# Kernel optimization log

Hardware: AMD Instinct MI355X
Metric: run time of the kernel (lower is better)

Reference implementation:

```python
import jax, jax.numpy as jnp
import numpy as np

N_NODES = 25000
N_EDGES = 800000
NUM_GRAPHS = 512
EMB = 128
OUT_EMB = 256
NUM_RADIAL = 6
NUM_DENSE = 3
NUM_TARGETS = 12


def setup_inputs() -> dict:
    key = jax.random.key(0)
    ks = jax.random.split(key, 10)
    m = jax.random.normal(ks[0], (N_EDGES, EMB), dtype=jnp.float32)
    rbf = jax.random.normal(ks[1], (N_EDGES, NUM_RADIAL), dtype=jnp.float32)
    edge_src = jax.random.randint(ks[2], (N_EDGES,), 0, N_NODES, dtype=jnp.int32)
    node2graph = jnp.sort(jax.random.randint(ks[3], (N_NODES,), 0, NUM_GRAPHS, dtype=jnp.int32))
    w_rbf = jax.random.normal(ks[4], (NUM_RADIAL, EMB), dtype=jnp.float32) * 0.4
    w_up = jax.random.normal(ks[5], (EMB, OUT_EMB), dtype=jnp.float32) * 0.08
    w_dense = jax.random.normal(ks[6], (NUM_DENSE, OUT_EMB, OUT_EMB), dtype=jnp.float32) * 0.06
    b_dense = jax.random.normal(ks[7], (NUM_DENSE, OUT_EMB), dtype=jnp.float32) * 0.01
    w_final = jax.random.normal(ks[8], (OUT_EMB, NUM_TARGETS), dtype=jnp.float32) * 0.05
    return {"m": m, "rbf": rbf, "edge_src": edge_src, "node2graph": node2graph,
            "w_rbf": w_rbf, "w_up": w_up, "w_dense": w_dense, "b_dense": b_dense,
            "w_final": w_final, "num_graphs": NUM_GRAPHS}


def reference(m, rbf, edge_src, node2graph, w_rbf, w_up, w_dense, b_dense, w_final, num_graphs):
    n_nodes = node2graph.shape[0]
    # edge: tmp = m * dense_rbf(rbf)   [E, emb]
    tmp = m * (rbf @ w_rbf)
    # reverse graph + copy_e/sum == scatter-sum per-edge tmp into original src node
    t = jax.ops.segment_sum(tmp, edge_src, num_segments=n_nodes)  # [N, emb]
    # up projection (no bias)
    t = t @ w_up  # [N, out_emb]
    # dense layers with swish activation
    for i in range(w_dense.shape[0]):
        t = jax.nn.silu(t @ w_dense[i] + b_dense[i])
    # final projection (no bias)
    t = t @ w_final  # [N, num_targets]
    # extensive readout: per-graph sum over nodes
    return jax.ops.segment_sum(t, node2graph, num_segments=num_graphs)  # [G, num_targets]
```

## Files before the change

### kernel.cpp

```cpp
#include <hip/hip_runtime.h>
#include <hip/hip_bf16.h>
#include <math.h>

#define EMB 128
#define OUT 256
#define RAD 6
#define NDL 3
#define NTGT 12
#define MT 32
#define S 264

typedef __attribute__((ext_vector_type(8))) short short8;
typedef __attribute__((ext_vector_type(4))) float floatx4;

__device__ inline short f2bf(float x) {
    __hip_bfloat16 h = __float2bfloat16(x);
    return *reinterpret_cast<short*>(&h);
}

__device__ inline unsigned pack2bf(float x, float y) {
    unsigned a = (unsigned short)f2bf(x);
    unsigned b = (unsigned short)f2bf(y);
    return a | (b << 16);
}


__global__ void hist_kernel(const int* __restrict__ src, int* __restrict__ counts, int E) {
    int i = blockIdx.x * blockDim.x + threadIdx.x;
    if (i < E) atomicAdd(&counts[src[i]], 1);
}

__global__ void scan_kernel(const int* __restrict__ counts, int* __restrict__ offs,
                            int* __restrict__ cursor, int N) {
    __shared__ int sums[1024];
    int tid = threadIdx.x;
    int chunk = (N + 1023) / 1024;
    int beg = tid * chunk;
    int end = min(beg + chunk, N);
    int s = 0;
    for (int i = beg; i < end; i++) s += counts[i];
    int mysum = s;
    sums[tid] = s;
    __syncthreads();
    for (int off = 1; off < 1024; off <<= 1) {
        int add = (tid >= off) ? sums[tid - off] : 0;
        __syncthreads();
        sums[tid] += add;
        __syncthreads();
    }
    int prefix = sums[tid] - mysum;
    for (int i = beg; i < end; i++) {
        int c = counts[i];
        offs[i] = prefix;
        cursor[i] = prefix;
        prefix += c;
    }
    if (tid == 0) offs[N] = sums[1023];
}

__global__ void scatter_kernel(const int* __restrict__ src, int* __restrict__ cursor,
                               int* __restrict__ eids, int E) {
    int i = blockIdx.x * blockDim.x + threadIdx.x;
    if (i < E) {
        int pos = atomicAdd(&cursor[src[i]], 1);
        eids[pos] = i;
    }
}


__global__ void prep_kernel(const float* __restrict__ w_up, const float* __restrict__ w_dense,
                            const float* __restrict__ w_final,
                            short* __restrict__ w_upT, short* __restrict__ w_dT,
                            short* __restrict__ w_fT) {
    const int T1 = OUT * EMB;
    const int T2 = NDL * OUT * OUT;
    const int T3 = 16 * OUT;
    int total = T1 + T2 + T3;
    for (int i = blockIdx.x * blockDim.x + threadIdx.x; i < total; i += gridDim.x * blockDim.x) {
        if (i < T1) {
            int n = i >> 7, k = i & 127;
            w_upT[i] = f2bf(w_up[k * OUT + n]);
        } else if (i < T1 + T2) {
            int j = i - T1;
            int l = j >> 16, o = (j >> 8) & 255, k = j & 255;
            w_dT[j] = f2bf(w_dense[(l << 16) + (k << 8) + o]);
        } else {
            int j = i - T1 - T2;
            int t = j >> 8, k = j & 255;
            w_fT[j] = (t < NTGT) ? f2bf(w_final[k * NTGT + t]) : (short)0;
        }
    }
}


__global__ __launch_bounds__(256) void fused_kernel(
    const float* __restrict__ m, const float* __restrict__ rbf,
    const float* __restrict__ w_rbf,
    const int* __restrict__ offs, const int* __restrict__ eids,
    const short* __restrict__ w_upT, const short* __restrict__ w_dT,
    const float* __restrict__ b_dense, const short* __restrict__ w_fT,
    const int* __restrict__ node2graph, float* __restrict__ out, int N) {

    __shared__ short sA[2][MT * S];

    const int tid = threadIdx.x;
    const int n0 = blockIdx.x * MT;
    const int wave = tid >> 6, lane = tid & 63;
    const int lo = lane & 15;
    const int quad = lane >> 4;
    const int kq = quad * 8;
    const int wcol = wave * 64;

    float2 wq[RAD];
#pragma unroll
    for (int r = 0; r < RAD; r++) wq[r] = *(const float2*)&w_rbf[r * EMB + 2 * lane];

#pragma unroll 1
    for (int s = 0; s < 8; s++) {
        const int r = wave * 8 + s;
        const int n = n0 + r;
        float ax = 0.f, ay = 0.f;
        if (n < N) {
            const int b = offs[n], e = offs[n + 1];
            int i = b;
            for (; i + 4 <= e; i += 4) {
                int ev[4];
                float2 mv[4];
                float2 rv[4][3];
#pragma unroll
                for (int j = 0; j < 4; j++) ev[j] = eids[i + j];
#pragma unroll
                for (int j = 0; j < 4; j++) {
                    const float* rb = &rbf[(size_t)ev[j] * RAD];
                    rv[j][0] = *(const float2*)&rb[0];
                    rv[j][1] = *(const float2*)&rb[2];
                    rv[j][2] = *(const float2*)&rb[4];
                    mv[j] = *(const float2*)&m[(size_t)ev[j] * EMB + 2 * lane];
                }
#pragma unroll
                for (int j = 0; j < 4; j++) {
                    float cx = wq[0].x * rv[j][0].x + wq[1].x * rv[j][0].y
                             + wq[2].x * rv[j][1].x + wq[3].x * rv[j][1].y
                             + wq[4].x * rv[j][2].x + wq[5].x * rv[j][2].y;
                    float cy = wq[0].y * rv[j][0].x + wq[1].y * rv[j][0].y
                             + wq[2].y * rv[j][1].x + wq[3].y * rv[j][1].y
                             + wq[4].y * rv[j][2].x + wq[5].y * rv[j][2].y;
                    ax += mv[j].x * cx;
                    ay += mv[j].y * cy;
                }
            }
            for (; i < e; i++) {
                int e0 = eids[i];
                const float* rb = &rbf[(size_t)e0 * RAD];
                float2 p0 = *(const float2*)&rb[0];
                float2 p1 = *(const float2*)&rb[2];
                float2 p2 = *(const float2*)&rb[4];
                float2 m0 = *(const float2*)&m[(size_t)e0 * EMB + 2 * lane];
                float cx = wq[0].x * p0.x + wq[1].x * p0.y + wq[2].x * p1.x
                         + wq[3].x * p1.y + wq[4].x * p2.x + wq[5].x * p2.y;
                float cy = wq[0].y * p0.x + wq[1].y * p0.y + wq[2].y * p1.x
                         + wq[3].y * p1.y + wq[4].y * p2.x + wq[5].y * p2.y;
                ax += m0.x * cx;
                ay += m0.y * cy;
            }
        }
        *(unsigned*)&sA[0][r * S + 2 * lane] = pack2bf(ax, ay);
    }
    __syncthreads();

    auto layer = [&](int cur, int K, const short* __restrict__ Bt,
                     const float* __restrict__ bias, bool act) {
        floatx4 acc[2][4];
#pragma unroll
        for (int mt = 0; mt < 2; mt++)
#pragma unroll
            for (int nt = 0; nt < 4; nt++)
                acc[mt][nt] = floatx4{0.f, 0.f, 0.f, 0.f};

        for (int kc = 0; kc < K; kc += 32) {
            short8 a0 = *(const short8*)&sA[cur][(lo) * S + kc + kq];
            short8 a1 = *(const short8*)&sA[cur][(16 + lo) * S + kc + kq];
#pragma unroll
            for (int nt = 0; nt < 4; nt++) {
                int n = wcol + nt * 16 + lo;
                short8 b = *(const short8*)&Bt[(size_t)n * K + kc + kq];
                acc[0][nt] = __builtin_amdgcn_mfma_f32_16x16x32_bf16(a0, b, acc[0][nt], 0, 0, 0);
                acc[1][nt] = __builtin_amdgcn_mfma_f32_16x16x32_bf16(a1, b, acc[1][nt], 0, 0, 0);
            }
        }

        float bv[4];
#pragma unroll
        for (int nt = 0; nt < 4; nt++) bv[nt] = bias ? bias[wcol + nt * 16 + lo] : 0.f;

        short* dst = sA[cur ^ 1];
#pragma unroll
        for (int mt = 0; mt < 2; mt++)
#pragma unroll
            for (int nt = 0; nt < 4; nt++) {
                int n = wcol + nt * 16 + lo;
#pragma unroll
                for (int i = 0; i < 4; i++) {
                    int mrow = mt * 16 + quad * 4 + i;
                    float x = acc[mt][nt][i] + bv[nt];
                    if (act) x = x / (1.f + __expf(-x));
                    dst[mrow * S + n] = f2bf(x);
                }
            }
        __syncthreads();
    };

    layer(0, EMB, w_upT, nullptr, false);
    layer(1, OUT, w_dT + 0 * OUT * OUT, b_dense + 0 * OUT, true);
    layer(0, OUT, w_dT + 1 * OUT * OUT, b_dense + 1 * OUT, true);
    layer(1, OUT, w_dT + 2 * OUT * OUT, b_dense + 2 * OUT, true);

    if (wave == 0) {
        floatx4 facc[2];
        facc[0] = floatx4{0.f, 0.f, 0.f, 0.f};
        facc[1] = floatx4{0.f, 0.f, 0.f, 0.f};
        for (int kc = 0; kc < OUT; kc += 32) {
            short8 a0 = *(const short8*)&sA[0][(lo) * S + kc + kq];
            short8 a1 = *(const short8*)&sA[0][(16 + lo) * S + kc + kq];
            short8 b = *(const short8*)&w_fT[lo * OUT + kc + kq];
            facc[0] = __builtin_amdgcn_mfma_f32_16x16x32_bf16(a0, b, facc[0], 0, 0, 0);
            facc[1] = __builtin_amdgcn_mfma_f32_16x16x32_bf16(a1, b, facc[1], 0, 0, 0);
        }
        if (lo < NTGT) {
#pragma unroll
            for (int mt = 0; mt < 2; mt++)
#pragma unroll
                for (int i = 0; i < 4; i++) {
                    int node = n0 + mt * 16 + quad * 4 + i;
                    if (node < N)
                        atomicAdd(&out[node2graph[node] * NTGT + lo], facc[mt][i]);
                }
        }
    }
}


extern "C" void kernel_launch(void* const* d_in, const int* in_sizes, int n_in,
                              void* d_out, int out_size, void* d_ws, size_t ws_size,
                              hipStream_t stream) {
    const float* m        = (const float*)d_in[0];
    const float* rbf      = (const float*)d_in[1];
    const int*   edge_src = (const int*)d_in[2];
    const int*   node2g   = (const int*)d_in[3];
    const float* w_rbf    = (const float*)d_in[4];
    const float* w_up     = (const float*)d_in[5];
    const float* w_dense  = (const float*)d_in[6];
    const float* b_dense  = (const float*)d_in[7];
    const float* w_final  = (const float*)d_in[8];

    int E = in_sizes[2];
    int N = in_sizes[3];
    float* out = (float*)d_out;

    char* p = (char*)d_ws;
    auto alloc = [&](size_t bytes) {
        char* r = p;
        p += (bytes + 255) & ~(size_t)255;
        return r;
    };
    int*   counts = (int*)alloc((size_t)N * 4);
    int*   offs   = (int*)alloc((size_t)(N + 1) * 4);
    int*   cursor = (int*)alloc((size_t)N * 4);
    int*   eids   = (int*)alloc((size_t)E * 4);
    short* w_upT  = (short*)alloc((size_t)OUT * EMB * 2);
    short* w_dT   = (short*)alloc((size_t)NDL * OUT * OUT * 2);
    short* w_fT   = (short*)alloc((size_t)16 * OUT * 2);

    hipMemsetAsync(counts, 0, (size_t)N * 4, stream);
    hipMemsetAsync(d_out, 0, (size_t)out_size * 4, stream);

    prep_kernel<<<512, 256, 0, stream>>>(w_up, w_dense, w_final, w_upT, w_dT, w_fT);
    hist_kernel<<<(E + 255) / 256, 256, 0, stream>>>(edge_src, counts, E);
    scan_kernel<<<1, 1024, 0, stream>>>(counts, offs, cursor, N);
    scatter_kernel<<<(E + 255) / 256, 256, 0, stream>>>(edge_src, cursor, eids, E);
    fused_kernel<<<(N + MT - 1) / MT, 256, 0, stream>>>(m, rbf, w_rbf, offs, eids,
                                                        w_upT, w_dT, b_dense, w_fT,
                                                        node2g, out, N);
}
```

Before: 811.7 us.

## Split fused kernel into per-node edge gather and separate MLP chain kernel

```diff
diff --git a/kernel.cpp b/kernel.cpp
--- a/kernel.cpp
+++ b/kernel.cpp
@@ -93,78 +93,139 @@
 }
 
 
-__global__ __launch_bounds__(256) void fused_kernel(
+__global__ __launch_bounds__(256) void gather_kernel(
     const float* __restrict__ m, const float* __restrict__ rbf,
     const float* __restrict__ w_rbf,
     const int* __restrict__ offs, const int* __restrict__ eids,
+    __hip_bfloat16* __restrict__ t0, int N) {
+
+    __shared__ float sRed[4][32][4];
+
+    const int n = blockIdx.x;
+    const int tid = threadIdx.x;
+    const int g = tid >> 5;
+    const int c = tid & 31;
+    const int wave = tid >> 6;
+
+    float4 wq[RAD];
+#pragma unroll
+    for (int r = 0; r < RAD; r++) wq[r] = *(const float4*)&w_rbf[r * EMB + 4 * c];
+
+    const int b = offs[n], e = offs[n + 1];
+    float ax = 0.f, ay = 0.f, az = 0.f, aw = 0.f;
+
+    int i = b + g;
+    for (; i + 24 < e; i += 32) {
+        int ev[4];
+        ev[0] = eids[i];
+        ev[1] = eids[i + 8];
+        ev[2] = eids[i + 16];
+        ev[3] = eids[i + 24];
+        float2 rv[4][3];
+        float4 mv[4];
+#pragma unroll
+        for (int j = 0; j < 4; j++) {
+            const float* rb = &rbf[(size_t)ev[j] * RAD];
+            rv[j][0] = *(const float2*)&rb[0];
+            rv[j][1] = *(const float2*)&rb[2];
+            rv[j][2] = *(const float2*)&rb[4];
+            mv[j] = *(const float4*)&m[(size_t)ev[j] * EMB + 4 * c];
+        }
+#pragma unroll
+        for (int j = 0; j < 4; j++) {
+            float cx = wq[0].x * rv[j][0].x + wq[1].x * rv[j][0].y
+                     + wq[2].x * rv[j][1].x + wq[3].x * rv[j][1].y
+                     + wq[4].x * rv[j][2].x + wq[5].x * rv[j][2].y;
+            float cy = wq[0].y * rv[j][0].x + wq[1].y * rv[j][0].y
+                     + wq[2].y * rv[j][1].x + wq[3].y * rv[j][1].y
+                     + wq[4].y * rv[j][2].x + wq[5].y * rv[j][2].y;
+            float cz = wq[0].z * rv[j][0].x + wq[1].z * rv[j][0].y
+                     + wq[2].z * rv[j][1].x + wq[3].z * rv[j][1].y
+                     + wq[4].z * rv[j][2].x + wq[5].z * rv[j][2].y;
+            float cw = wq[0].w * rv[j][0].x + wq[1].w * rv[j][0].y
+                     + wq[2].w * rv[j][1].x + wq[3].w * rv[j][1].y
+                     + wq[4].w * rv[j][2].x + wq[5].w * rv[j][2].y;
+            ax += mv[j].x * cx;
+            ay += mv[j].y * cy;
+            az += mv[j].z * cz;
+            aw += mv[j].w * cw;
+        }
+    }
+    for (; i < e; i += 8) {
+        int e0 = eids[i];
+        const float* rb = &rbf[(size_t)e0 * RAD];
+        float2 p0 = *(const float2*)&rb[0];
+        float2 p1 = *(const float2*)&rb[2];
+        float2 p2 = *(const float2*)&rb[4];
+        float4 m0 = *(const float4*)&m[(size_t)e0 * EMB + 4 * c];
+        float cx = wq[0].x * p0.x + wq[1].x * p0.y + wq[2].x * p1.x
+                 + wq[3].x * p1.y + wq[4].x * p2.x + wq[5].x * p2.y;
+        float cy = wq[0].y * p0.x + wq[1].y * p0.y + wq[2].y * p1.x
+                 + wq[3].y * p1.y + wq[4].y * p2.x + wq[5].y * p2.y;
+        float cz = wq[0].z * p0.x + wq[1].z * p0.y + wq[2].z * p1.x
+                 + wq[3].z * p1.y + wq[4].z * p2.x + wq[5].z * p2.y;
+        float cw = wq[0].w * p0.x + wq[1].w * p0.y + wq[2].w * p1.x
+                 + wq[3].w * p1.y + wq[4].w * p2.x + wq[5].w * p2.y;
+        ax += m0.x * cx;
+        ay += m0.y * cy;
+        az += m0.z * cz;
+        aw += m0.w * cw;
+    }
+
+    ax += __shfl_xor(ax, 32);
+    ay += __shfl_xor(ay, 32);
+    az += __shfl_xor(az, 32);
+    aw += __shfl_xor(aw, 32);
+
+    if ((tid & 63) < 32) {
+        float4 v = {ax, ay, az, aw};
+        *(float4*)&sRed[wave][c][0] = v;
+    }
+    __syncthreads();
+    if (tid < 32) {
+        float4 v0 = *(const float4*)&sRed[0][c][0];
+        float4 v1 = *(const float4*)&sRed[1][c][0];
+        float4 v2 = *(const float4*)&sRed[2][c][0];
+        float4 v3 = *(const float4*)&sRed[3][c][0];
+        float rx = v0.x + v1.x + v2.x + v3.x;
+        float ry = v0.y + v1.y + v2.y + v3.y;
+        float rz = v0.z + v1.z + v2.z + v3.z;
+        float rw = v0.w + v1.w + v2.w + v3.w;
+        unsigned lo = pack2bf(rx, ry);
+        unsigned hi = pack2bf(rz, rw);
+        uint2 pk = {lo, hi};
+        *(uint2*)((short*)t0 + (size_t)n * EMB + 4 * c) = pk;
+    }
+}
+
+
+__global__ __launch_bounds__(256) void chain_kernel(
+    const __hip_bfloat16* __restrict__ t0,
     const short* __restrict__ w_upT, const short* __restrict__ w_dT,
     const float* __restrict__ b_dense, const short* __restrict__ w_fT,
     const int* __restrict__ node2graph, float* __restrict__ out, int N) {
 
     __shared__ short sA[2][MT * S];
 
-    const int tid = threadIdx.x;
-    const int n0 = blockIdx.x * MT;
-    const int wave = tid >> 6, lane = tid & 63;
-    const int lo = lane & 15;
-    const int quad = lane >> 4;
-    const int kq = quad * 8;
-    const int wcol = wave * 64;
-
-    float2 wq[RAD];
-#pragma unroll
-    for (int r = 0; r < RAD; r++) wq[r] = *(const float2*)&w_rbf[r * EMB + 2 * lane];
-
-#pragma unroll 1
-    for (int s = 0; s < 8; s++) {
-        const int r = wave * 8 + s;
-        const int n = n0 + r;
-        float ax = 0.f, ay = 0.f;
-        if (n < N) {
-            const int b = offs[n], e = offs[n + 1];
-            int i = b;
-            for (; i + 4 <= e; i += 4) {
-                int ev[4];
-                float2 mv[4];
-                float2 rv[4][3];
-#pragma unroll
-                for (int j = 0; j < 4; j++) ev[j] = eids[i + j];
-#pragma unroll
-                for (int j = 0; j < 4; j++) {
-                    const float* rb = &rbf[(size_t)ev[j] * RAD];
-                    rv[j][0] = *(const float2*)&rb[0];
-                    rv[j][1] = *(const float2*)&rb[2];
-                    rv[j][2] = *(const float2*)&rb[4];
-                    mv[j] = *(const float2*)&m[(size_t)ev[j] * EMB + 2 * lane];
-                }
-#pragma unroll
-                for (int j = 0; j < 4; j++) {
-                    float cx = wq[0].x * rv[j][0].x + wq[1].x * rv[j][0].y
-                             + wq[2].x * rv[j][1].x + wq[3].x * rv[j][1].y
-                             + wq[4].x * rv[j][2].x + wq[5].x * rv[j][2].y;
-                    float cy = wq[0].y * rv[j][0].x + wq[1].y * rv[j][0].y
-                             + wq[2].y * rv[j][1].x + wq[3].y * rv[j][1].y
-                             + wq[4].y * rv[j][2].x + wq[5].y * rv[j][2].y;
-                    ax += mv[j].x * cx;
-                    ay += mv[j].y * cy;
-                }
-            }
-            for (; i < e; i++) {
-                int e0 = eids[i];
-                const float* rb = &rbf[(size_t)e0 * RAD];
-                float2 p0 = *(const float2*)&rb[0];
-                float2 p1 = *(const float2*)&rb[2];
-                float2 p2 = *(const float2*)&rb[4];
-                float2 m0 = *(const float2*)&m[(size_t)e0 * EMB + 2 * lane];
-                float cx = wq[0].x * p0.x + wq[1].x * p0.y + wq[2].x * p1.x
-                         + wq[3].x * p1.y + wq[4].x * p2.x + wq[5].x * p2.y;
-                float cy = wq[0].y * p0.x + wq[1].y * p0.y + wq[2].y * p1.x
-                         + wq[3].y * p1.y + wq[4].y * p2.x + wq[5].y * p2.y;
-                ax += m0.x * cx;
-                ay += m0.y * cy;
-            }
-        }
-        *(unsigned*)&sA[0][r * S + 2 * lane] = pack2bf(ax, ay);
+    int tid = threadIdx.x;
+    int n0 = blockIdx.x * MT;
+    int wave = tid >> 6, lane = tid & 63;
+    int lo = lane & 15;
+    int quad = lane >> 4;
+    int kq = quad * 8;
+    int wcol = wave * 64;
+
+    {
+        int r = tid >> 3;
+        int c = (tid & 7) * 16;
+        uint4 v0 = {0, 0, 0, 0}, v1 = {0, 0, 0, 0};
+        if (n0 + r < N) {
+            const uint4* src = (const uint4*)((const short*)t0 + (size_t)(n0 + r) * EMB + c);
+            v0 = src[0];
+            v1 = src[1];
+        }
+        *(uint4*)&sA[0][r * S + c] = v0;
+        *(uint4*)&sA[0][r * S + c + 8] = v1;
     }
     __syncthreads();
 
@@ -267,6 +328,7 @@
     int*   offs   = (int*)alloc((size_t)(N + 1) * 4);
     int*   cursor = (int*)alloc((size_t)N * 4);
     int*   eids   = (int*)alloc((size_t)E * 4);
+    __hip_bfloat16* t0 = (__hip_bfloat16*)alloc((size_t)N * EMB * 2);
     short* w_upT  = (short*)alloc((size_t)OUT * EMB * 2);
     short* w_dT   = (short*)alloc((size_t)NDL * OUT * OUT * 2);
     short* w_fT   = (short*)alloc((size_t)16 * OUT * 2);
@@ -278,7 +340,7 @@
     hist_kernel<<<(E + 255) / 256, 256, 0, stream>>>(edge_src, counts, E);
     scan_kernel<<<1, 1024, 0, stream>>>(counts, offs, cursor, N);
     scatter_kernel<<<(E + 255) / 256, 256, 0, stream>>>(edge_src, cursor, eids, E);
-    fused_kernel<<<(N + MT - 1) / MT, 256, 0, stream>>>(m, rbf, w_rbf, offs, eids,
-                                                        w_upT, w_dT, b_dense, w_fT,
-                                                        node2g, out, N);
-}
+    gather_kernel<<<N, 256, 0, stream>>>(m, rbf, w_rbf, offs, eids, t0, N);
+    chain_kernel<<<(N + MT - 1) / MT, 256, 0, stream>>>(t0, w_upT, w_dT, b_dense,
+                                                        w_fT, node2g, out, N);
+}
```

Result: faster. 779.7 us (-3.9%).

## Replace CSR sort-based gather with atomic scatter-add into fp32 node buffer

Applied to the files above, without the earlier changes.

```diff
diff --git a/kernel.cpp b/kernel.cpp
--- a/kernel.cpp
+++ b/kernel.cpp
@@ -22,49 +22,6 @@
     unsigned a = (unsigned short)f2bf(x);
     unsigned b = (unsigned short)f2bf(y);
     return a | (b << 16);
-}
-
-
-__global__ void hist_kernel(const int* __restrict__ src, int* __restrict__ counts, int E) {
-    int i = blockIdx.x * blockDim.x + threadIdx.x;
-    if (i < E) atomicAdd(&counts[src[i]], 1);
-}
-
-__global__ void scan_kernel(const int* __restrict__ counts, int* __restrict__ offs,
-                            int* __restrict__ cursor, int N) {
-    __shared__ int sums[1024];
-    int tid = threadIdx.x;
-    int chunk = (N + 1023) / 1024;
-    int beg = tid * chunk;
-    int end = min(beg + chunk, N);
-    int s = 0;
-    for (int i = beg; i < end; i++) s += counts[i];
-    int mysum = s;
-    sums[tid] = s;
-    __syncthreads();
-    for (int off = 1; off < 1024; off <<= 1) {
-        int add = (tid >= off) ? sums[tid - off] : 0;
-        __syncthreads();
-        sums[tid] += add;
-        __syncthreads();
-    }
-    int prefix = sums[tid] - mysum;
-    for (int i = beg; i < end; i++) {
-        int c = counts[i];
-        offs[i] = prefix;
-        cursor[i] = prefix;
-        prefix += c;
-    }
-    if (tid == 0) offs[N] = sums[1023];
-}
-
-__global__ void scatter_kernel(const int* __restrict__ src, int* __restrict__ cursor,
-                               int* __restrict__ eids, int E) {
-    int i = blockIdx.x * blockDim.x + threadIdx.x;
-    if (i < E) {
-        int pos = atomicAdd(&cursor[src[i]], 1);
-        eids[pos] = i;
-    }
 }
 
 
@@ -93,78 +50,98 @@
 }
 
 
-__global__ __launch_bounds__(256) void fused_kernel(
+__global__ __launch_bounds__(256) void edge_kernel(
     const float* __restrict__ m, const float* __restrict__ rbf,
-    const float* __restrict__ w_rbf,
-    const int* __restrict__ offs, const int* __restrict__ eids,
+    const float* __restrict__ w_rbf, const int* __restrict__ edge_src,
+    float* __restrict__ t0, int E) {
+
+    const int lane = threadIdx.x & 63;
+    const int wave = threadIdx.x >> 6;
+
+    float2 wq[RAD];
+#pragma unroll
+    for (int r = 0; r < RAD; r++) wq[r] = *(const float2*)&w_rbf[r * EMB + 2 * lane];
+
+    const int base = (blockIdx.x * 4 + wave) * 4;
+    if (base >= E) return;
+
+    if (base + 4 <= E) {
+        int sv[4];
+        float2 mv[4];
+        float2 r0[4], r1[4], r2[4];
+#pragma unroll
+        for (int j = 0; j < 4; j++) sv[j] = edge_src[base + j];
+#pragma unroll
+        for (int j = 0; j < 4; j++) {
+            const float* rb = &rbf[(size_t)(base + j) * RAD];
+            r0[j] = *(const float2*)&rb[0];
+            r1[j] = *(const float2*)&rb[2];
+            r2[j] = *(const float2*)&rb[4];
+            mv[j] = *(const float2*)&m[(size_t)(base + j) * EMB + 2 * lane];
+        }
+#pragma unroll
+        for (int j = 0; j < 4; j++) {
+            float cx = wq[0].x * r0[j].x + wq[1].x * r0[j].y
+                     + wq[2].x * r1[j].x + wq[3].x * r1[j].y
+                     + wq[4].x * r2[j].x + wq[5].x * r2[j].y;
+            float cy = wq[0].y * r0[j].x + wq[1].y * r0[j].y
+                     + wq[2].y * r1[j].x + wq[3].y * r1[j].y
+                     + wq[4].y * r2[j].x + wq[5].y * r2[j].y;
+            float* dst = &t0[(size_t)sv[j] * EMB + 2 * lane];
+            atomicAdd(&dst[0], mv[j].x * cx);
+            atomicAdd(&dst[1], mv[j].y * cy);
+        }
+    } else {
+        for (int i = base; i < E; i++) {
+            int s0 = edge_src[i];
+            const float* rb = &rbf[(size_t)i * RAD];
+            float2 p0 = *(const float2*)&rb[0];
+            float2 p1 = *(const float2*)&rb[2];
+            float2 p2 = *(const float2*)&rb[4];
+            float2 m0 = *(const float2*)&m[(size_t)i * EMB + 2 * lane];
+            float cx = wq[0].x * p0.x + wq[1].x * p0.y + wq[2].x * p1.x
+                     + wq[3].x * p1.y + wq[4].x * p2.x + wq[5].x * p2.y;
+            float cy = wq[0].y * p0.x + wq[1].y * p0.y + wq[2].y * p1.x
+                     + wq[3].y * p1.y + wq[4].y * p2.x + wq[5].y * p2.y;
+            float* dst = &t0[(size_t)s0 * EMB + 2 * lane];
+            atomicAdd(&dst[0], m0.x * cx);
+            atomicAdd(&dst[1], m0.y * cy);
+        }
+    }
+}
+
+
+__global__ __launch_bounds__(256) void chain_kernel(
+    const float* __restrict__ t0,
     const short* __restrict__ w_upT, const short* __restrict__ w_dT,
     const float* __restrict__ b_dense, const short* __restrict__ w_fT,
     const int* __restrict__ node2graph, float* __restrict__ out, int N) {
 
     __shared__ short sA[2][MT * S];
 
-    const int tid = threadIdx.x;
-    const int n0 = blockIdx.x * MT;
-    const int wave = tid >> 6, lane = tid & 63;
-    const int lo = lane & 15;
-    const int quad = lane >> 4;
-    const int kq = quad * 8;
-    const int wcol = wave * 64;
-
-    float2 wq[RAD];
-#pragma unroll
-    for (int r = 0; r < RAD; r++) wq[r] = *(const float2*)&w_rbf[r * EMB + 2 * lane];
-
-#pragma unroll 1
-    for (int s = 0; s < 8; s++) {
-        const int r = wave * 8 + s;
-        const int n = n0 + r;
-        float ax = 0.f, ay = 0.f;
-        if (n < N) {
-            const int b = offs[n], e = offs[n + 1];
-            int i = b;
-            for (; i + 4 <= e; i += 4) {
-                int ev[4];
-                float2 mv[4];
-                float2 rv[4][3];
-#pragma unroll
-                for (int j = 0; j < 4; j++) ev[j] = eids[i + j];
-#pragma unroll
-                for (int j = 0; j < 4; j++) {
-                    const float* rb = &rbf[(size_t)ev[j] * RAD];
-                    rv[j][0] = *(const float2*)&rb[0];
-                    rv[j][1] = *(const float2*)&rb[2];
-                    rv[j][2] = *(const float2*)&rb[4];
-                    mv[j] = *(const float2*)&m[(size_t)ev[j] * EMB + 2 * lane];
-                }
-#pragma unroll
-                for (int j = 0; j < 4; j++) {
-                    float cx = wq[0].x * rv[j][0].x + wq[1].x * rv[j][0].y
-                             + wq[2].x * rv[j][1].x + wq[3].x * rv[j][1].y
-                             + wq[4].x * rv[j][2].x + wq[5].x * rv[j][2].y;
-                    float cy = wq[0].y * rv[j][0].x + wq[1].y * rv[j][0].y
-                             + wq[2].y * rv[j][1].x + wq[3].y * rv[j][1].y
-                             + wq[4].y * rv[j][2].x + wq[5].y * rv[j][2].y;
-                    ax += mv[j].x * cx;
-                    ay += mv[j].y * cy;
-                }
-            }
-            for (; i < e; i++) {
-                int e0 = eids[i];
-                const float* rb = &rbf[(size_t)e0 * RAD];
-                float2 p0 = *(const float2*)&rb[0];
-                float2 p1 = *(const float2*)&rb[2];
-                float2 p2 = *(const float2*)&rb[4];
-                float2 m0 = *(const float2*)&m[(size_t)e0 * EMB + 2 * lane];
-                float cx = wq[0].x * p0.x + wq[1].x * p0.y + wq[2].x * p1.x
-                         + wq[3].x * p1.y + wq[4].x * p2.x + wq[5].x * p2.y;
-                float cy = wq[0].y * p0.x + wq[1].y * p0.y + wq[2].y * p1.x
-                         + wq[3].y * p1.y + wq[4].y * p2.x + wq[5].y * p2.y;
-                ax += m0.x * cx;
-                ay += m0.y * cy;
-            }
-        }
-        *(unsigned*)&sA[0][r * S + 2 * lane] = pack2bf(ax, ay);
+    int tid = threadIdx.x;
+    int n0 = blockIdx.x * MT;
+    int wave = tid >> 6, lane = tid & 63;
+    int lo = lane & 15;
+    int quad = lane >> 4;
+    int kq = quad * 8;
+    int wcol = wave * 64;
+
+    {
+        int r = tid >> 3;
+        int c = (tid & 7) * 16;
+        float4 v0 = {0, 0, 0, 0}, v1 = v0, v2 = v0, v3 = v0;
+        if (n0 + r < N) {
+            const float4* src = (const float4*)(t0 + (size_t)(n0 + r) * EMB + c);
+            v0 = src[0]; v1 = src[1]; v2 = src[2]; v3 = src[3];
+        }
+        uint4 pk0, pk1;
+        pk0.x = pack2bf(v0.x, v0.y); pk0.y = pack2bf(v0.z, v0.w);
+        pk0.z = pack2bf(v1.x, v1.y); pk0.w = pack2bf(v1.z, v1.w);
+        pk1.x = pack2bf(v2.x, v2.y); pk1.y = pack2bf(v2.z, v2.w);
+        pk1.z = pack2bf(v3.x, v3.y); pk1.w = pack2bf(v3.z, v3.w);
+        *(uint4*)&sA[0][r * S + c] = pk0;
+        *(uint4*)&sA[0][r * S + c + 8] = pk1;
     }
     __syncthreads();
 
@@ -263,22 +240,16 @@
         p += (bytes + 255) & ~(size_t)255;
         return r;
     };
-    int*   counts = (int*)alloc((size_t)N * 4);
-    int*   offs   = (int*)alloc((size_t)(N + 1) * 4);
-    int*   cursor = (int*)alloc((size_t)N * 4);
-    int*   eids   = (int*)alloc((size_t)E * 4);
+    float* t0     = (float*)alloc((size_t)N * EMB * 4);
     short* w_upT  = (short*)alloc((size_t)OUT * EMB * 2);
     short* w_dT   = (short*)alloc((size_t)NDL * OUT * OUT * 2);
     short* w_fT   = (short*)alloc((size_t)16 * OUT * 2);
 
-    hipMemsetAsync(counts, 0, (size_t)N * 4, stream);
+    hipMemsetAsync(t0, 0, (size_t)N * EMB * 4, stream);
     hipMemsetAsync(d_out, 0, (size_t)out_size * 4, stream);
 
     prep_kernel<<<512, 256, 0, stream>>>(w_up, w_dense, w_final, w_upT, w_dT, w_fT);
-    hist_kernel<<<(E + 255) / 256, 256, 0, stream>>>(edge_src, counts, E);
-    scan_kernel<<<1, 1024, 0, stream>>>(counts, offs, cursor, N);
-    scatter_kernel<<<(E + 255) / 256, 256, 0, stream>>>(edge_src, cursor, eids, E);
-    fused_kernel<<<(N + MT - 1) / MT, 256, 0, stream>>>(m, rbf, w_rbf, offs, eids,
-                                                        w_upT, w_dT, b_dense, w_fT,
-                                                        node2g, out, N);
-}
+    edge_kernel<<<(E + 15) / 16, 256, 0, stream>>>(m, rbf, w_rbf, edge_src, t0, E);
+    chain_kernel<<<(N + MT - 1) / MT, 256, 0, stream>>>(t0, w_upT, w_dT, b_dense,
+                                                        w_fT, node2g, out, N);
+}
```

Measured after the change: 1.142 ms. 1.41x slower.
